# Optimization experiments

Hardware: AMD Instinct MI355X
Metric: run time of the kernel (lower is better)

Reference implementation:

```python
import jax, jax.numpy as jnp
import numpy as np

N_USER = 20000
N_ITEM = 20000
N = N_USER + N_ITEM          # total nodes
D = 128                      # n_hid (= in_feats = out_feats)
H = 4                        # GAT heads
L = 2                        # n_layers
M = 8                        # mem_size (hypernet bottleneck)
T = 5                        # num_rels in MemoryLayer
E_UI = 40000                 # user->item bipartite edges
E_T = 16000                  # homogeneous edges per relation type (grouped)
EPS = 1e-5


def _layer_norm(x, w, b):
    mu = x.mean(-1, keepdims=True)
    var = ((x - mu) ** 2).mean(-1, keepdims=True)
    return (x - mu) * jax.lax.rsqrt(var + EPS) * w + b


def _gat(h_src, h_dst, src_idx, dst_idx, n_dst, W, al, ar, bias):
    """DGL GATConv (shared fc, eval-mode dropout=identity, elu activation)."""
    fs = (h_src @ W.T).reshape(-1, H, D)          # [Ns, H, D]
    fd = (h_dst @ W.T).reshape(-1, H, D)          # [Nd, H, D]
    el = (fs * al).sum(-1)                        # [Ns, H]
    er = (fd * ar).sum(-1)                        # [Nd, H]
    e = jax.nn.leaky_relu(el[src_idx] + er[dst_idx], 0.2)   # [E, H]
    emax = jax.ops.segment_max(e, dst_idx, num_segments=n_dst)
    ex = jnp.exp(e - emax[dst_idx])
    denom = jax.ops.segment_sum(ex, dst_idx, num_segments=n_dst)
    a = ex / denom[dst_idx]                       # edge softmax per dst
    rst = jax.ops.segment_sum(a[:, :, None] * fs[src_idx], dst_idx, num_segments=n_dst)
    return jax.nn.elu(rst + bias.reshape(1, H, D))           # [Nd, H, D]


def _memory_layer(feat, edge_src, edge_dst, Wc, bc, Ww, nWc, nbc, nWw, h_bias, ln_w, ln_b):
    # edges grouped by relation type: edge_src/edge_dst are [T, E_T]
    hs = feat[edge_src]                           # [T, Et, D]
    hd = feat[edge_dst]                           # [T, Et, D]
    # per-edge hypernetwork: coef = LeakyReLU(Linear(dst)); w = Ww(coef); msg = w @ src
    coef = jax.nn.leaky_relu(jnp.einsum('ted,tmd->tem', hd, Wc) + bc[:, None, :], 0.2)
    tmp = jnp.einsum('tei,tmoi->temo', hs, Ww)    # [T, Et, M, D] -- M-bottleneck path
    msg = jnp.einsum('tem,temo->teo', coef, tmp)  # [T, Et, D]
    flat_dst = edge_dst.reshape(-1)
    s = jax.ops.segment_sum(msg.reshape(-1, D), flat_dst, num_segments=N)
    cnt = jax.ops.segment_sum(jnp.ones((flat_dst.shape[0],), feat.dtype), flat_dst, num_segments=N)
    agg = s / jnp.maximum(cnt, 1.0)[:, None]      # fn.mean (0 for isolated nodes)
    rep = _layer_norm(agg, ln_w, ln_b) + h_bias
    # self-loop node_ME(feat, feat)
    ncoef = jax.nn.leaky_relu(feat @ nWc.T + nbc, 0.2)       # [N, M]
    ntmp = jnp.einsum('ni,moi->nmo', feat, nWw)              # [N, M, D]
    rep = rep + jnp.einsum('nm,nmo->no', ncoef, ntmp)
    return jax.nn.leaky_relu(rep, 0.2)            # dropout = identity (eval)


def setup_inputs() -> dict:
    key = jax.random.key(0)
    ks = jax.random.split(key, 16)
    s = 0.05
    return {
        "embedding": jax.random.normal(ks[0], (N, D), jnp.float32),
        "gat_fc_W": jax.random.normal(ks[1], (L, 2, H * D, D), jnp.float32) * s,
        "gat_attn_l": jax.random.normal(ks[2], (L, 2, H, D), jnp.float32) * s,
        "gat_attn_r": jax.random.normal(ks[3], (L, 2, H, D), jnp.float32) * s,
        "gat_bias": jnp.zeros((L, 2, H * D), jnp.float32),
        "proj_W": jax.random.normal(ks[4], (L, 2, D, H * D), jnp.float32) * s,
        "proj_b": jnp.zeros((L, 2, D), jnp.float32),
        "mem_rel_Wc": jax.random.normal(ks[5], (L, T, M, D), jnp.float32) * s,
        "mem_rel_bc": jnp.zeros((L, T, M), jnp.float32),
        "mem_rel_Ww": jax.random.normal(ks[6], (L, T, M, D, D), jnp.float32) * s,
        "mem_node_Wc": jax.random.normal(ks[7], (L, M, D), jnp.float32) * s,
        "mem_node_bc": jnp.zeros((L, M), jnp.float32),
        "mem_node_Ww": jax.random.normal(ks[8], (L, M, D, D), jnp.float32) * s,
        "mem_h_bias": jnp.zeros((L, D), jnp.float32),
        "mem_ln_w": jnp.ones((L, D), jnp.float32),
        "mem_ln_b": jnp.zeros((L, D), jnp.float32),
        "final_ln_w": jnp.ones(((L + 1) * D,), jnp.float32),
        "final_ln_b": jnp.zeros(((L + 1) * D,), jnp.float32),
        "src_u": jax.random.randint(ks[9], (E_UI,), 0, N_USER, jnp.int32),
        "dst_i": jax.random.randint(ks[10], (E_UI,), 0, N_ITEM, jnp.int32),
        "edge_src": jax.random.randint(ks[11], (T, E_T), 0, N, jnp.int32),
        "edge_dst": jax.random.randint(ks[12], (T, E_T), 0, N, jnp.int32),
    }


def reference(embedding, gat_fc_W, gat_attn_l, gat_attn_r, gat_bias, proj_W, proj_b,
              mem_rel_Wc, mem_rel_bc, mem_rel_Ww, mem_node_Wc, mem_node_bc, mem_node_Ww,
              mem_h_bias, mem_ln_w, mem_ln_b, final_ln_w, final_ln_b,
              src_u, dst_i, edge_src, edge_dst):
    features = embedding
    all_emb = [features]
    for l in range(L):
        hu, hi = features[:N_USER], features[N_USER:]
        # relation 0: item -> user (dst = user)
        gu = _gat(hi, hu, dst_i, src_u, N_USER,
                  gat_fc_W[l, 0], gat_attn_l[l, 0], gat_attn_r[l, 0], gat_bias[l, 0])
        ru = jax.nn.elu(gu.reshape(N_USER, H * D) @ proj_W[l, 0].T + proj_b[l, 0])
        # relation 1: user -> item (dst = item)
        gi = _gat(hu, hi, src_u, dst_i, N_ITEM,
                  gat_fc_W[l, 1], gat_attn_l[l, 1], gat_attn_r[l, 1], gat_bias[l, 1])
        ri = jnp.asarray(jax.nn.elu(gi.reshape(N_ITEM, H * D) @ proj_W[l, 1].T + proj_b[l, 1]))
        trans = jnp.concatenate([ru, ri], axis=0)             # [N, D]
        mem = _memory_layer(all_emb[-1], edge_src, edge_dst,
                            mem_rel_Wc[l], mem_rel_bc[l], mem_rel_Ww[l],
                            mem_node_Wc[l], mem_node_bc[l], mem_node_Ww[l],
                            mem_h_bias[l], mem_ln_w[l], mem_ln_b[l])
        features = mem + trans
        all_emb.append(features)
    return _layer_norm(jnp.concatenate(all_emb, axis=1), final_ln_w, final_ln_b)
```

## Files before the change

### kernel.cpp

```cpp
#include <hip/hip_runtime.h>
#include <hip/hip_bf16.h>
#include <math.h>

typedef __hip_bfloat16 bf16;

#define NUSER 20000
#define NITEM 20000
#define NTOT  40000
#define DD    128
#define HH    4
#define TT    5
#define MMEM  8
#define EUI   40000
#define ET    16000

#define MP_N  40064
#define MP_H  20096

typedef __attribute__((ext_vector_type(8))) short short8;
typedef __attribute__((ext_vector_type(4))) float f32x4;

__device__ __forceinline__ void gload16(const bf16* g, bf16* l){
  __builtin_amdgcn_global_load_lds(
      (const __attribute__((address_space(1))) unsigned int*)g,
      (__attribute__((address_space(3))) unsigned int*)l, 16, 0, 0);
}
__device__ __forceinline__ float bu2f_lo(unsigned u){ return __uint_as_float(u << 16); }
__device__ __forceinline__ float bu2f_hi(unsigned u){ return __uint_as_float(u & 0xffff0000u); }

__device__ __forceinline__ int stage_cg(int lane){
  return (((lane&3) ^ ((lane>>2)&3) ^ (lane>>4)) << 3);
}
__device__ __forceinline__ int read_pc8(int lm, int lq){
  return ((lq ^ (lm&3) ^ ((lm>>2)&3)) << 3);
}

__global__ __launch_bounds__(256) void k_mfma_gemm(
    const bf16* __restrict__ A, const bf16* __restrict__ B,
    const float* __restrict__ bias, float* __restrict__ C,
    long Astr, long Bstr, long biasStr, long Cstr,
    int ldc, int M, int K, int act, int accum)
{
  A += (size_t)blockIdx.z*Astr; B += (size_t)blockIdx.z*Bstr;
  if (bias) bias += (size_t)blockIdx.z*biasStr;
  C += (size_t)blockIdx.z*Cstr;
  __shared__ bf16 As[3][4096];
  __shared__ bf16 Bs[3][4096];
  int tid = threadIdx.x;
  int wave = tid >> 6, lane = tid & 63;
  int r0 = blockIdx.x * 128, c0 = blockIdx.y * 128;
  int wm = (wave >> 1) * 64, wn = (wave & 1) * 64;
  f32x4 acc[4][4];
  #pragma unroll
  for (int i=0;i<4;i++)
    #pragma unroll
    for (int j=0;j<4;j++) acc[i][j] = (f32x4){0.f,0.f,0.f,0.f};

  int rq = lane >> 2;
  int cg = stage_cg(lane);
  const bf16* Ag = A + (size_t)(r0 + wave*32 + rq)*K + cg;
  const bf16* Bg = B + (size_t)(c0 + wave*32 + rq)*K + cg;
  int lm = lane & 15, lq = lane >> 4;
  int pc8 = read_pc8(lm, lq);

  int ns = K >> 5;
  {
    bf16* dA = &As[0][wave*1024]; bf16* dB = &Bs[0][wave*1024];
    gload16(Ag,        dA); gload16(Ag + 16*K, dA + 512);
    gload16(Bg,        dB); gload16(Bg + 16*K, dB + 512);
  }
  if (ns > 1){
    bf16* dA = &As[1][wave*1024]; bf16* dB = &Bs[1][wave*1024];
    gload16(Ag + 32,        dA); gload16(Ag + 16*K + 32, dA + 512);
    gload16(Bg + 32,        dB); gload16(Bg + 16*K + 32, dB + 512);
    asm volatile("s_waitcnt vmcnt(4)" ::: "memory");
  } else {
    asm volatile("s_waitcnt vmcnt(0)" ::: "memory");
  }
  __builtin_amdgcn_s_barrier();

  int cur = 0, stg = 2;
  for (int i = 0; i < ns; i++){
    if (i + 2 < ns){
      int k2 = (i + 2) << 5;
      bf16* dA = &As[stg][wave*1024]; bf16* dB = &Bs[stg][wave*1024];
      gload16(Ag + k2,        dA); gload16(Ag + 16*K + k2, dA + 512);
      gload16(Bg + k2,        dB); gload16(Bg + 16*K + k2, dB + 512);
    }
    const bf16* Ard = &As[cur][(wm + lm)*32 + pc8];
    const bf16* Brd = &Bs[cur][(wn + lm)*32 + pc8];
    short8 af[4], bfv[4];
    #pragma unroll
    for (int ii=0;ii<4;ii++) af[ii]  = *(const short8*)(Ard + ii*16*32);
    #pragma unroll
    for (int j=0;j<4;j++)    bfv[j]  = *(const short8*)(Brd + j*16*32);
    #pragma unroll
    for (int ii=0;ii<4;ii++)
      #pragma unroll
      for (int j=0;j<4;j++)
        acc[ii][j] = __builtin_amdgcn_mfma_f32_16x16x32_bf16(af[ii], bfv[j], acc[ii][j], 0, 0, 0);
    if (i < ns - 1){
      if (i + 2 < ns) asm volatile("s_waitcnt vmcnt(4)" ::: "memory");
      else            asm volatile("s_waitcnt vmcnt(0)" ::: "memory");
      __builtin_amdgcn_s_barrier();
    }
    cur = (cur == 2) ? 0 : cur + 1;
    stg = (stg == 2) ? 0 : stg + 1;
  }
  #pragma unroll
  for (int i=0;i<4;i++){
    #pragma unroll
    for (int j=0;j<4;j++){
      int c = c0 + wn + j*16 + lm;
      #pragma unroll
      for (int rg=0; rg<4; rg++){
        int r = r0 + wm + i*16 + lq*4 + rg;
        if (r < M){
          float v = acc[i][j][rg];
          if (bias) v += bias[c];
          if (act==1) v = v>0.f ? v : expm1f(v);
          float* cp = &C[(size_t)r*ldc + c];
          if (accum) *cp += v; else *cp = v;
        }
      }
    }
  }
}

__global__ __launch_bounds__(256) void k_fc_gemm(
    const bf16* __restrict__ A, const bf16* __restrict__ B,
    bf16* __restrict__ Fb, const float* __restrict__ al, const float* __restrict__ ar,
    float* __restrict__ el, float* __restrict__ er, int M)
{
  __shared__ bf16 As[128*32];
  __shared__ bf16 Bs[128*32];
  __shared__ float redE[2][2][128];
  int tid = threadIdx.x;
  int wave = tid >> 6, lane = tid & 63;
  int h = blockIdx.y;
  int r0 = blockIdx.x * 128;
  int wm = (wave >> 1) * 64, wn = (wave & 1) * 64;
  f32x4 acc[4][4];
  #pragma unroll
  for (int i=0;i<4;i++)
    #pragma unroll
    for (int j=0;j<4;j++) acc[i][j] = (f32x4){0.f,0.f,0.f,0.f};

  int rq = lane >> 2;
  int cg = stage_cg(lane);
  const bf16* Ag = A + (size_t)(r0 + wave*32 + rq)*128 + cg;
  const bf16* Bg = B + (size_t)(h*128 + wave*32 + rq)*128 + cg;
  bf16* AsW = As + wave*32*32;
  bf16* BsW = Bs + wave*32*32;
  int lm = lane & 15, lq = lane >> 4;
  int pc8 = read_pc8(lm, lq);
  const bf16* Ard = As + (wm + lm)*32 + pc8;
  const bf16* Brd = Bs + (wn + lm)*32 + pc8;

  for (int k0 = 0; k0 < 128; k0 += 32){
    gload16(Ag + k0,             AsW);
    gload16(Ag + 16*128 + k0,    AsW + 16*32);
    gload16(Bg + k0,             BsW);
    gload16(Bg + 16*128 + k0,    BsW + 16*32);
    __syncthreads();
    short8 af[4], bfv[4];
    #pragma unroll
    for (int i=0;i<4;i++) af[i]  = *(const short8*)(Ard + i*16*32);
    #pragma unroll
    for (int j=0;j<4;j++) bfv[j] = *(const short8*)(Brd + j*16*32);
    #pragma unroll
    for (int i=0;i<4;i++)
      #pragma unroll
      for (int j=0;j<4;j++)
        acc[i][j] = __builtin_amdgcn_mfma_f32_16x16x32_bf16(af[i], bfv[j], acc[i][j], 0, 0, 0);
    __syncthreads();
  }
  float alv[4], arv[4];
  #pragma unroll
  for (int j=0;j<4;j++){
    int c = h*128 + wn + j*16 + lm;
    alv[j] = al[c]; arv[j] = ar[c];
  }
  int wnh = wave & 1;
  #pragma unroll
  for (int i=0;i<4;i++){
    #pragma unroll
    for (int rg=0; rg<4; rg++){
      float se = 0.f, sr = 0.f;
      #pragma unroll
      for (int j=0;j<4;j++){
        float v = acc[i][j][rg];
        se = fmaf(v, alv[j], se);
        sr = fmaf(v, arv[j], sr);
      }
      #pragma unroll
      for (int msk=1; msk<16; msk<<=1){
        se += __shfl_xor(se, msk);
        sr += __shfl_xor(sr, msk);
      }
      if (lm == 0){
        int rl = wm + i*16 + lq*4 + rg;
        redE[0][wnh][rl] = se;
        redE[1][wnh][rl] = sr;
      }
    }
  }
  #pragma unroll
  for (int i=0;i<4;i++){
    #pragma unroll
    for (int j=0;j<4;j++){
      int c = h*128 + wn + j*16 + lm;
      #pragma unroll
      for (int rg=0; rg<4; rg++){
        int r = r0 + wm + i*16 + lq*4 + rg;
        if (r < M) Fb[(size_t)r*512 + c] = __float2bfloat16(acc[i][j][rg]);
      }
    }
  }
  __syncthreads();
  if (tid < 128){
    int r = r0 + tid;
    if (r < M) el[(size_t)r*4 + h] = redE[0][0][tid] + redE[0][1][tid];
  } else {
    int t2 = tid - 128;
    int r = r0 + t2;
    if (r < M) er[(size_t)r*4 + h] = redE[1][0][t2] + redE[1][1][t2];
  }
}

__global__ __launch_bounds__(256) void k_memgemm(
    const float* __restrict__ feat, const int* __restrict__ src,
    const float* __restrict__ coef, const bf16* __restrict__ B,
    float* __restrict__ C, bf16* __restrict__ Cb,
    const float* __restrict__ trans, float* __restrict__ fout,
    long srcStr, long coefStr, long Bstr, long CbStr,
    int Mvalid, int mode)
{
  __shared__ bf16 Af[64*136];
  __shared__ float cfS[8*64];
  __shared__ bf16 Bs[3][2][4096];
  int t = blockIdx.y;
  const int*   srcT  = src ? src + (size_t)t*srcStr : nullptr;
  const float* coefT = coef + (size_t)t*coefStr;
  const bf16*  Bt    = B + (size_t)t*Bstr;
  int tid = threadIdx.x, wave = tid >> 6, lane = tid & 63;
  int r0 = blockIdx.x * 64;

  {
    int rL = tid >> 2, seg = tid & 3;
    int r = r0 + rL;
    bool valid = r < Mvalid;
    int s = valid ? (srcT ? srcT[r] : r) : 0;
    const float4* fp = (const float4*)(feat + (size_t)s*128 + seg*32);
    bf16* ap = Af + rL*136 + seg*32;
    #pragma unroll
    for (int q=0;q<8;q+=2){
      float4 v0 = fp[q], v1 = fp[q+1];
      *(__hip_bfloat162*)(ap + q*4)     = __float22bfloat162_rn(make_float2(v0.x, v0.y));
      *(__hip_bfloat162*)(ap + q*4 + 2) = __float22bfloat162_rn(make_float2(v0.z, v0.w));
      *(__hip_bfloat162*)(ap + q*4 + 4) = __float22bfloat162_rn(make_float2(v1.x, v1.y));
      *(__hip_bfloat162*)(ap + q*4 + 6) = __float22bfloat162_rn(make_float2(v1.z, v1.w));
    }
  }
  if (tid < 64){
    int r = r0 + tid;
    bool valid = r < Mvalid;
    #pragma unroll
    for (int m=0;m<8;m++)
      cfS[m*64 + tid] = valid ? coefT[(size_t)r*8 + m] : 0.f;
  }

  int rq = lane >> 2;
  int cg = stage_cg(lane);
  const bf16* Bg0 = Bt + (size_t)(wave*32 + rq)*1024 + cg;
  const bf16* Bg1 = Bt + (size_t)(wave*32 + 16 + rq)*1024 + cg;
  int wm = (wave >> 1) * 32, wn = (wave & 1) * 64;
  int lm = lane & 15, lq = lane >> 4;
  int pc8 = read_pc8(lm, lq);

  #pragma unroll
  for (int p0=0; p0<2; p0++){
    #pragma unroll
    for (int h=0; h<2; h++){
      int kk = p0*2 + h;
      bf16* d = &Bs[p0][h][wave*1024];
      gload16(Bg0 + kk*32, d);
      gload16(Bg1 + kk*32, d + 512);
    }
  }
  asm volatile("s_waitcnt lgkmcnt(0) vmcnt(4)" ::: "memory");
  __builtin_amdgcn_s_barrier();

  short8 afr[4][2];
  #pragma unroll
  for (int ic=0; ic<4; ic++)
    #pragma unroll
    for (int i=0; i<2; i++)
      afr[ic][i] = *(const short8*)(Af + (size_t)(wm + i*16 + lm)*136 + ic*32 + lq*8);

  f32x4 accC[2][4];
  #pragma unroll
  for (int i=0;i<2;i++)
    #pragma unroll
    for (int j=0;j<4;j++) accC[i][j] = (f32x4){0.f,0.f,0.f,0.f};
  f32x4 accM[2][4];

  #pragma unroll
  for (int p = 0; p < 16; p++){
    if (p + 2 < 16){
      #pragma unroll
      for (int h=0; h<2; h++){
        const int kk = (p+2)*2 + h;
        bf16* d = &Bs[(p+2)%3][h][wave*1024];
        gload16(Bg0 + kk*32, d);
        gload16(Bg1 + kk*32, d + 512);
      }
    }
    #pragma unroll
    for (int h=0; h<2; h++){
      const int kk = p*2 + h;
      const int ic = kk & 3;
      const bf16* bb = &Bs[p%3][h][0];
      short8 bfv[4];
      #pragma unroll
      for (int j=0;j<4;j++)
        bfv[j] = *(const short8*)(bb + (wn + lm + j*16)*32 + pc8);
      if (ic == 0){
        #pragma unroll
        for (int i=0;i<2;i++)
          #pragma unroll
          for (int j=0;j<4;j++)
            accM[i][j] = __builtin_amdgcn_mfma_f32_16x16x32_bf16(afr[0][i], bfv[j],
                             (f32x4){0.f,0.f,0.f,0.f}, 0, 0, 0);
      } else {
        #pragma unroll
        for (int i=0;i<2;i++)
          #pragma unroll
          for (int j=0;j<4;j++)
            accM[i][j] = __builtin_amdgcn_mfma_f32_16x16x32_bf16(afr[ic][i], bfv[j], accM[i][j], 0, 0, 0);
      }
    }
    if (p & 1){
      const int m = p >> 1;
      #pragma unroll
      for (int i=0;i<2;i++){
        f32x4 cf4 = *(const f32x4*)(cfS + m*64 + wm + i*16 + lq*4);
        #pragma unroll
        for (int j=0;j<4;j++)
          #pragma unroll
          for (int rg=0; rg<4; rg++)
            accC[i][j][rg] = fmaf(cf4[rg], accM[i][j][rg], accC[i][j][rg]);
      }
    }
    if (p < 15){
      if (p + 2 < 16) asm volatile("s_waitcnt vmcnt(4)" ::: "memory");
      else            asm volatile("s_waitcnt vmcnt(0)" ::: "memory");
      __builtin_amdgcn_s_barrier();
    }
  }

  #pragma unroll
  for (int i=0;i<2;i++){
    #pragma unroll
    for (int j=0;j<4;j++){
      int c = wn + j*16 + lm;
      #pragma unroll
      for (int rg=0; rg<4; rg++){
        int r = r0 + wm + i*16 + lq*4 + rg;
        if (r < Mvalid){
          float v = accC[i][j][rg];
          if (mode == 0){
            Cb[(size_t)t*CbStr + (size_t)r*128 + c] = __float2bfloat16(v);
          } else {
            float x = C[(size_t)r*128 + c] + v;
            x = x>0.f ? x : 0.2f*x;
            fout[(size_t)r*128 + c] = x + trans[(size_t)r*128 + c];
          }
        }
      }
    }
  }
}

__global__ void k_f2b(const float* __restrict__ in, bf16* __restrict__ o, int nv, int nt){
  int i = blockIdx.x*256 + threadIdx.x;
  if (i < nt) o[i] = __float2bfloat16(i < nv ? in[i] : 0.f);
}

__global__ void k_repack(const float* __restrict__ in, bf16* __restrict__ o){
  int s = blockIdx.y;
  int g = blockIdx.x*256 + threadIdx.x;
  int m = g >> 14, od = (g >> 7) & 127, i = g & 127;
  o[(size_t)s*131072 + (size_t)od*1024 + m*128 + i] = __float2bfloat16(in[(size_t)s*131072 + g]);
}

__global__ void k_hist(const int* __restrict__ dIdx, int* __restrict__ cnt, int E){
  int e = blockIdx.x*256+threadIdx.x;
  if (e<E) atomicAdd(&cnt[dIdx[e]], 1);
}

__global__ __launch_bounds__(1024) void k_scan(const int* __restrict__ in,
                                               int* __restrict__ out, int n){
  __shared__ int wsum[16];
  __shared__ int carry;
  int tidx = threadIdx.x, lane = tidx & 63, w = tidx >> 6;
  if (tidx == 0) carry = 0;
  __syncthreads();
  for (int base = 0; base < n; base += 1024){
    int i = base + tidx;
    int v = (i < n) ? in[i] : 0;
    int x = v;
    #pragma unroll
    for (int off = 1; off < 64; off <<= 1){
      int t = __shfl_up(x, off);
      if (lane >= off) x += t;
    }
    if (lane == 63) wsum[w] = x;
    __syncthreads();
    if (w == 0 && lane < 16){
      int t = wsum[lane];
      #pragma unroll
      for (int off=1; off<16; off<<=1){
        int u = __shfl_up(t, off, 16);
        if (lane >= off) t += u;
      }
      wsum[lane] = t;
    }
    __syncthreads();
    int woff = (w == 0) ? 0 : wsum[w-1];
    int excl = carry + woff + x - v;
    if (i < n) out[i] = excl;
    __syncthreads();
    if (tidx == 1023) carry = carry + wsum[15];
    __syncthreads();
  }
  if (tidx == 0) out[n] = carry;
}

__global__ void k_csr_scatter(const int* __restrict__ sIdx, const int* __restrict__ dIdx,
                              int sOff, const int* __restrict__ rowptr,
                              int* __restrict__ cursor, int* __restrict__ col, int E){
  int e = blockIdx.x*256+threadIdx.x; if (e>=E) return;
  int d = dIdx[e];
  int pos = rowptr[d] + atomicAdd(&cursor[d], 1);
  col[pos] = sIdx[e] + sOff;
}

__global__ void k_csr_scatter_eid(const int* __restrict__ dIdx, const int* __restrict__ rowptr,
                                  int* __restrict__ cursor, int* __restrict__ col, int E){
  int e = blockIdx.x*256+threadIdx.x; if (e>=E) return;
  int d = dIdx[e];
  int pos = rowptr[d] + atomicAdd(&cursor[d], 1);
  col[pos] = e;
}

__global__ __launch_bounds__(64) void k_gat_gather(
    const int* __restrict__ rowptr, const int* __restrict__ col,
    const float* __restrict__ el, const float* __restrict__ er,
    const bf16* __restrict__ Fb, const float* __restrict__ gb,
    bf16* __restrict__ rstb, int dOff)
{
  int dl = blockIdx.x;
  int lane = threadIdx.x;
  int h = lane >> 4;
  int off = (lane & 15) << 3;
  float erh = er[(size_t)(dl + dOff)*4 + h];
  float m = -INFINITY, den = 0.f;
  float acc[8];
  #pragma unroll
  for (int i=0;i<8;i++) acc[i]=0.f;
  int jb = rowptr[dl], je = rowptr[dl+1];
  for (int j=jb; j<je; j++){
    int s = col[j];
    float e = el[(size_t)s*4+h] + erh;
    e = e > 0.f ? e : 0.2f*e;
    float mn = fmaxf(m, e);
    float sc = __expf(m - mn);
    float wj = __expf(e - mn);
    den = den*sc + wj;
    m = mn;
    uint4 u = *(const uint4*)(Fb + (size_t)s*512 + h*128 + off);
    acc[0]=acc[0]*sc + wj*bu2f_lo(u.x); acc[1]=acc[1]*sc + wj*bu2f_hi(u.x);
    acc[2]=acc[2]*sc + wj*bu2f_lo(u.y); acc[3]=acc[3]*sc + wj*bu2f_hi(u.y);
    acc[4]=acc[4]*sc + wj*bu2f_lo(u.z); acc[5]=acc[5]*sc + wj*bu2f_hi(u.z);
    acc[6]=acc[6]*sc + wj*bu2f_lo(u.w); acc[7]=acc[7]*sc + wj*bu2f_hi(u.w);
  }
  float inv = den > 0.f ? 1.f/den : 0.f;
  int cb = h*128 + off;
  float x[8];
  #pragma unroll
  for (int q=0;q<8;q++){
    float v = acc[q]*inv + gb[cb+q];
    x[q] = v>0.f ? v : expm1f(v);
  }
  union { uint4 u; __hip_bfloat162 p[4]; } O;
  #pragma unroll
  for (int q=0;q<4;q++) O.p[q] = __float22bfloat162_rn(make_float2(x[2*q], x[2*q+1]));
  *(uint4*)(rstb + (size_t)dl*512 + cb) = O.u;
}

__global__ void k_coef(const float* __restrict__ feat, const int* __restrict__ idx,
                       const float* __restrict__ Wc, const float* __restrict__ bc,
                       float* __restrict__ outc, int cnt){
  int t = blockIdx.y;
  __shared__ float wT[DD*MMEM];
  __shared__ float bS[MMEM];
  for (int i=threadIdx.x;i<MMEM*DD;i+=128){
    int m = i >> 7, d = i & 127;
    wT[d*MMEM + m] = Wc[(size_t)t*MMEM*DD + i];
  }
  if (threadIdx.x < MMEM) bS[threadIdx.x] = bc[t*MMEM + threadIdx.x];
  __syncthreads();
  int e = blockIdx.x*128 + threadIdx.x; if (e >= cnt) return;
  int node = idx ? idx[(size_t)t*cnt + e] : e;
  float acc[MMEM];
  #pragma unroll
  for (int m=0;m<MMEM;m++) acc[m]=bS[m];
  const float4* fr = (const float4*)(feat + (size_t)node*DD);
  for (int d4=0; d4<32; d4++){
    float4 v = fr[d4];
    const float* w0 = wT + d4*4*MMEM;
    #pragma unroll
    for (int m=0;m<MMEM;m++) acc[m] = fmaf(v.x, w0[m], acc[m]);
    #pragma unroll
    for (int m=0;m<MMEM;m++) acc[m] = fmaf(v.y, w0[MMEM+m], acc[m]);
    #pragma unroll
    for (int m=0;m<MMEM;m++) acc[m] = fmaf(v.z, w0[2*MMEM+m], acc[m]);
    #pragma unroll
    for (int m=0;m<MMEM;m++) acc[m] = fmaf(v.w, w0[3*MMEM+m], acc[m]);
  }
  float* op = outc + ((size_t)t*cnt + e)*MMEM;
  #pragma unroll
  for (int m=0;m<MMEM;m++){ float v=acc[m]; op[m] = v>0.f ? v : 0.2f*v; }
}

__global__ void k_mem_gather(const int* __restrict__ rpT, const int* __restrict__ colT,
                             const bf16* __restrict__ msg, float* __restrict__ sAgg){
  int n = blockIdx.x*4 + (threadIdx.x >> 6);
  if (n >= NTOT) return;
  int lane = threadIdx.x & 63;
  int jb = rpT[n], je = rpT[n+1];
  float a0=0.f, a1=0.f;
  for (int j=jb;j<je;j++){
    unsigned u = ((const unsigned*)(msg + (size_t)colT[j]*128))[lane];
    a0 += bu2f_lo(u); a1 += bu2f_hi(u);
  }
  *(float2*)(sAgg + (size_t)n*128 + lane*2) = make_float2(a0, a1);
}

__global__ void k_memln(const float* __restrict__ s, const int* __restrict__ rpT,
                        const float* __restrict__ lw, const float* __restrict__ lb,
                        const float* __restrict__ hb, float* __restrict__ outp){
  int n = blockIdx.x, lane = threadIdx.x;
  float c = fmaxf((float)(rpT[n+1]-rpT[n]), 1.f);
  float x1 = s[(size_t)n*128+lane]/c, x2 = s[(size_t)n*128+64+lane]/c;
  float t = x1+x2;
  #pragma unroll
  for (int off=32;off;off>>=1) t += __shfl_xor(t,off);
  float mu = t * (1.f/128.f);
  float d1=x1-mu, d2=x2-mu;
  float v = d1*d1+d2*d2;
  #pragma unroll
  for (int off=32;off;off>>=1) v += __shfl_xor(v,off);
  float r = rsqrtf(v*(1.f/128.f) + 1e-5f);
  outp[(size_t)n*128+lane]    = d1*r*lw[lane]    + lb[lane]    + hb[lane];
  outp[(size_t)n*128+64+lane] = d2*r*lw[64+lane] + lb[64+lane] + hb[64+lane];
}

__global__ void k_final_ln(const float* __restrict__ emb, const float* __restrict__ f1,
                           const float* __restrict__ f2, const float* __restrict__ w,
                           const float* __restrict__ b, float* __restrict__ out){
  int n = blockIdx.x, t = threadIdx.x;
  __shared__ float red[4];
  float x0 = emb[(size_t)n*128+t];
  float x1 = f1[(size_t)n*128+t];
  float x2 = f2[(size_t)n*128+t];
  float s = x0+x1+x2;
  #pragma unroll
  for (int off=32;off;off>>=1) s += __shfl_xor(s,off);
  if ((t&63)==0) red[t>>6] = s;
  __syncthreads();
  float mu = (red[0]+red[1]) * (1.f/384.f);
  float d0=x0-mu, d1=x1-mu, d2=x2-mu;
  float v = d0*d0+d1*d1+d2*d2;
  #pragma unroll
  for (int off=32;off;off>>=1) v += __shfl_xor(v,off);
  if ((t&63)==0) red[2+(t>>6)] = v;
  __syncthreads();
  float var = (red[2]+red[3]) * (1.f/384.f);
  float r = rsqrtf(var + 1e-5f);
  size_t o = (size_t)n*384;
  out[o+t]     = d0*r*w[t]     + b[t];
  out[o+128+t] = d1*r*w[128+t] + b[128+t];
  out[o+256+t] = d2*r*w[256+t] + b[256+t];
}

extern "C" void kernel_launch(void* const* d_in, const int* in_sizes, int n_in,
                              void* d_out, int out_size, void* d_ws, size_t ws_size,
                              hipStream_t stream)
{
  const float* emb   = (const float*)d_in[0];
  const float* fcW   = (const float*)d_in[1];
  const float* attl  = (const float*)d_in[2];
  const float* attr  = (const float*)d_in[3];
  const float* gbias = (const float*)d_in[4];
  const float* projW = (const float*)d_in[5];
  const float* projB = (const float*)d_in[6];
  const float* relWc = (const float*)d_in[7];
  const float* relbc = (const float*)d_in[8];
  const float* relWw = (const float*)d_in[9];
  const float* nodWc = (const float*)d_in[10];
  const float* nodbc = (const float*)d_in[11];
  const float* nodWw = (const float*)d_in[12];
  const float* hbias = (const float*)d_in[13];
  const float* mlnw  = (const float*)d_in[14];
  const float* mlnb  = (const float*)d_in[15];
  const float* flnw  = (const float*)d_in[16];
  const float* flnb  = (const float*)d_in[17];
  const int*  srcU  = (const int*)d_in[18];
  const int*  dstI  = (const int*)d_in[19];
  const int*  eSrc  = (const int*)d_in[20];
  const int*  eDst  = (const int*)d_in[21];
  float* out = (float*)d_out;

  char* wp = (char*)d_ws;
  auto alloc = [&](size_t bytes)->void* {
    void* p = (void*)wp; wp += (bytes + 511) & ~(size_t)511; return p;
  };
  float* feat1 = (float*)alloc((size_t)NTOT*DD*4);
  float* feat2 = (float*)alloc((size_t)NTOT*DD*4);
  float* Fbuf  = (float*)alloc((size_t)NTOT*512*4);
  float* rst   = (float*)alloc((size_t)NTOT*DD*2*4);
  bf16*  rstb0 = (bf16*)alloc((size_t)2*MP_H*512*2);
  float* trans = (float*)alloc((size_t)NTOT*DD*4);
  float* elF   = (float*)alloc((size_t)NTOT*4*4);
  float* erF   = (float*)alloc((size_t)NTOT*4*4);
  int* rpA  = (int*)alloc((size_t)(NUSER+1)*4);
  int* colA = (int*)alloc((size_t)EUI*4);
  int* rpB  = (int*)alloc((size_t)(NITEM+1)*4);
  int* colB = (int*)alloc((size_t)EUI*4);
  int* icnt = (int*)alloc((size_t)20000*4);
  int* icur = (int*)alloc((size_t)20000*4);
  int* rpT  = (int*)alloc((size_t)(NTOT+1)*4);
  int* colT = (int*)alloc((size_t)TT*ET*4);
  int* cntT = (int*)alloc((size_t)NTOT*4);
  int* icurT= (int*)alloc((size_t)NTOT*4);
  bf16* featb  = (bf16*)alloc((size_t)MP_N*DD*2);
  bf16* fcWb   = (bf16*)alloc((size_t)4*512*DD*2);
  bf16* projWb = (bf16*)alloc((size_t)4*DD*512*2);
  bf16* relWwb = (bf16*)alloc((size_t)10*DD*1024*2);
  bf16* nodWwb = (bf16*)alloc((size_t)2*DD*1024*2);
  bf16*  Fb     = (bf16*)Fbuf;
  bf16*  msgBb  = (bf16*)((char*)Fbuf + (size_t)NTOT*512*2);
  float* coefB  = (float*)((char*)msgBb + (size_t)TT*ET*128*2);
  float* ncoefB = coefB + (size_t)TT*ET*8;
  bf16*  rstb1  = rstb0 + (size_t)MP_H*512;
  float* sAgg   = rst;
  float* memO   = rst + (size_t)NTOT*DD;

  k_f2b<<<dim3((4*512*DD+255)/256),256,0,stream>>>(fcW, fcWb, 4*512*DD, 4*512*DD);
  k_f2b<<<dim3((4*DD*512+255)/256),256,0,stream>>>(projW, projWb, 4*DD*512, 4*DD*512);
  k_repack<<<dim3(512,10),256,0,stream>>>(relWw, relWwb);
  k_repack<<<dim3(512,2),256,0,stream>>>(nodWw, nodWwb);
  hipMemsetAsync(rstb0 + (size_t)20000*512, 0, (size_t)(MP_H-20000)*512*2, stream);
  hipMemsetAsync(rstb1 + (size_t)20000*512, 0, (size_t)(MP_H-20000)*512*2, stream);

  hipMemsetAsync(icnt, 0, 20000*4, stream);
  hipMemsetAsync(icur, 0, 20000*4, stream);
  k_hist<<<dim3((EUI+255)/256),256,0,stream>>>(srcU, icnt, EUI);
  k_scan<<<dim3(1),1024,0,stream>>>(icnt, rpA, NUSER);
  k_csr_scatter<<<dim3((EUI+255)/256),256,0,stream>>>(dstI, srcU, NUSER, rpA, icur, colA, EUI);
  hipMemsetAsync(icnt, 0, 20000*4, stream);
  hipMemsetAsync(icur, 0, 20000*4, stream);
  k_hist<<<dim3((EUI+255)/256),256,0,stream>>>(dstI, icnt, EUI);
  k_scan<<<dim3(1),1024,0,stream>>>(icnt, rpB, NITEM);
  k_csr_scatter<<<dim3((EUI+255)/256),256,0,stream>>>(srcU, dstI, 0, rpB, icur, colB, EUI);
  hipMemsetAsync(cntT, 0, NTOT*4, stream);
  hipMemsetAsync(icurT, 0, NTOT*4, stream);
  k_hist<<<dim3((TT*ET+255)/256),256,0,stream>>>(eDst, cntT, TT*ET);
  k_scan<<<dim3(1),1024,0,stream>>>(cntT, rpT, NTOT);
  k_csr_scatter_eid<<<dim3((TT*ET+255)/256),256,0,stream>>>(eDst, rpT, icurT, colT, TT*ET);

  const float* feats[3] = {emb, feat1, feat2};
  for (int l=0; l<2; l++){
    const float* fin  = feats[l];
    float* fout = (float*)feats[l+1];

    k_f2b<<<dim3((MP_N*DD+255)/256),256,0,stream>>>(fin, featb, NTOT*DD, MP_N*DD);

    for (int d=0; d<2; d++){
      k_fc_gemm<<<dim3(MP_N/128, 4),256,0,stream>>>(
          featb, fcWb + (size_t)(l*2+d)*512*DD, Fb,
          attl+(size_t)(l*2+d)*512, attr+(size_t)(l*2+d)*512, elF, erF, NTOT);
      int dOff = (d==0) ? 0 : NUSER;
      const int* rp  = (d==0) ? rpA : rpB;
      const int* col = (d==0) ? colA : colB;
      k_gat_gather<<<dim3(20000),64,0,stream>>>(rp, col, elF, erF, Fb,
          gbias+(size_t)(l*2+d)*512, (d==0) ? rstb0 : rstb1, dOff);
    }
    k_mfma_gemm<<<dim3(MP_H/128, 1, 2),256,0,stream>>>(
        rstb0, projWb + (size_t)(l*2)*DD*512, projB + (size_t)(l*2)*DD, trans,
        (long)MP_H*512, (long)DD*512, (long)DD, (long)20000*DD,
        DD, 20000, 512, 1, 0);

    k_coef<<<dim3((ET+127)/128, TT),128,0,stream>>>(fin, eDst,
        relWc+(size_t)l*TT*MMEM*DD, relbc+(size_t)l*TT*MMEM, coefB, ET);
    k_memgemm<<<dim3(ET/64, TT),256,0,stream>>>(
        fin, eSrc, coefB, relWwb + (size_t)l*TT*DD*1024,
        nullptr, msgBb, nullptr, nullptr,
        (long)ET, (long)ET*8, (long)DD*1024, (long)ET*128, ET, 0);
    k_mem_gather<<<dim3(NTOT/4),256,0,stream>>>(rpT, colT, msgBb, sAgg);
    k_memln<<<dim3(NTOT),64,0,stream>>>(sAgg, rpT, mlnw+(size_t)l*DD, mlnb+(size_t)l*DD,
                                        hbias+(size_t)l*DD, memO);
    k_coef<<<dim3((NTOT+127)/128, 1),128,0,stream>>>(fin, nullptr,
        nodWc+(size_t)l*MMEM*DD, nodbc+(size_t)l*MMEM, ncoefB, NTOT);
    k_memgemm<<<dim3(MP_N/64, 1),256,0,stream>>>(
        fin, nullptr, ncoefB, nodWwb + (size_t)l*DD*1024,
        memO, nullptr, trans, fout,
        0, 0, 0, 0, NTOT, 2);
  }

  k_final_ln<<<dim3(NTOT),128,0,stream>>>(emb, feat1, feat2, flnw, flnb, out);
}
```

Baseline: 894.3 us.

## Triple-buffer LDS staging in GAT fc GEMM to overlap loads with MFMA

The k-loop of the fc GEMM kernel now uses three LDS buffers, prefetching the tile two steps ahead with async global-to-LDS loads. Explicit vmcnt waits and raw barriers replace the per-iteration double __syncthreads. The goal is to hide global load latency behind MFMA work. In exchange the kernel uses more LDS, which can lower occupancy, and with only four k-steps the prefetch has little room to pay off.

```diff
diff --git a/kernel.cpp b/kernel.cpp
--- a/kernel.cpp
+++ b/kernel.cpp
@@ -132,8 +132,8 @@
     bf16* __restrict__ Fb, const float* __restrict__ al, const float* __restrict__ ar,
     float* __restrict__ el, float* __restrict__ er, int M)
 {
-  __shared__ bf16 As[128*32];
-  __shared__ bf16 Bs[128*32];
+  __shared__ bf16 As[3][4096];
+  __shared__ bf16 Bs[3][4096];
   __shared__ float redE[2][2][128];
   int tid = threadIdx.x;
   int wave = tid >> 6, lane = tid & 63;
@@ -150,30 +150,47 @@
   int cg = stage_cg(lane);
   const bf16* Ag = A + (size_t)(r0 + wave*32 + rq)*128 + cg;
   const bf16* Bg = B + (size_t)(h*128 + wave*32 + rq)*128 + cg;
-  bf16* AsW = As + wave*32*32;
-  bf16* BsW = Bs + wave*32*32;
   int lm = lane & 15, lq = lane >> 4;
   int pc8 = read_pc8(lm, lq);
-  const bf16* Ard = As + (wm + lm)*32 + pc8;
-  const bf16* Brd = Bs + (wn + lm)*32 + pc8;
-
-  for (int k0 = 0; k0 < 128; k0 += 32){
-    gload16(Ag + k0,             AsW);
-    gload16(Ag + 16*128 + k0,    AsW + 16*32);
-    gload16(Bg + k0,             BsW);
-    gload16(Bg + 16*128 + k0,    BsW + 16*32);
-    __syncthreads();
+
+  {
+    bf16* dA = &As[0][wave*1024]; bf16* dB = &Bs[0][wave*1024];
+    gload16(Ag,            dA); gload16(Ag + 16*128, dA + 512);
+    gload16(Bg,            dB); gload16(Bg + 16*128, dB + 512);
+  }
+  {
+    bf16* dA = &As[1][wave*1024]; bf16* dB = &Bs[1][wave*1024];
+    gload16(Ag + 32,       dA); gload16(Ag + 16*128 + 32, dA + 512);
+    gload16(Bg + 32,       dB); gload16(Bg + 16*128 + 32, dB + 512);
+  }
+  asm volatile("s_waitcnt vmcnt(4)" ::: "memory");
+  __builtin_amdgcn_s_barrier();
+
+  #pragma unroll
+  for (int i = 0; i < 4; i++){
+    if (i + 2 < 4){
+      const int k2 = (i + 2) << 5;
+      bf16* dA = &As[(i+2)%3][wave*1024]; bf16* dB = &Bs[(i+2)%3][wave*1024];
+      gload16(Ag + k2,        dA); gload16(Ag + 16*128 + k2, dA + 512);
+      gload16(Bg + k2,        dB); gload16(Bg + 16*128 + k2, dB + 512);
+    }
+    const bf16* Ard = &As[i%3][(wm + lm)*32 + pc8];
+    const bf16* Brd = &Bs[i%3][(wn + lm)*32 + pc8];
     short8 af[4], bfv[4];
     #pragma unroll
-    for (int i=0;i<4;i++) af[i]  = *(const short8*)(Ard + i*16*32);
-    #pragma unroll
-    for (int j=0;j<4;j++) bfv[j] = *(const short8*)(Brd + j*16*32);
-    #pragma unroll
-    for (int i=0;i<4;i++)
+    for (int ii=0;ii<4;ii++) af[ii]  = *(const short8*)(Ard + ii*16*32);
+    #pragma unroll
+    for (int j=0;j<4;j++)    bfv[j]  = *(const short8*)(Brd + j*16*32);
+    #pragma unroll
+    for (int ii=0;ii<4;ii++)
       #pragma unroll
       for (int j=0;j<4;j++)
-        acc[i][j] = __builtin_amdgcn_mfma_f32_16x16x32_bf16(af[i], bfv[j], acc[i][j], 0, 0, 0);
-    __syncthreads();
+        acc[ii][j] = __builtin_amdgcn_mfma_f32_16x16x32_bf16(af[ii], bfv[j], acc[ii][j], 0, 0, 0);
+    if (i < 3){
+      if (i + 2 < 4) asm volatile("s_waitcnt vmcnt(4)" ::: "memory");
+      else           asm volatile("s_waitcnt vmcnt(0)" ::: "memory");
+      __builtin_amdgcn_s_barrier();
+    }
   }
   float alv[4], arv[4];
   #pragma unroll
```

After: 899.6 us. Within noise of the previous version (+0.6%).
